# Performance work log

Hardware: AMD Instinct MI355X
Metric: run time of the kernel (lower is better)

## Reference

```python
import jax, jax.numpy as jnp
import numpy as np

# Tree config: batch of perfect binary trees in heap layout (root=0, children of i are 2i+1, 2i+2)
D_MODEL = 512
DEPTH = 10                      # number of internal levels
B = 64                          # number of trees in the batch
VOCAB = 32000
N_LEAVES = 2 ** DEPTH           # 1024 leaves per tree
N_NODES = 2 ** (DEPTH + 1) - 1  # 2047 nodes per tree
N_CLASSES = 2                   # binary graph classification


def setup_inputs() -> dict:
    key = jax.random.key(0)
    k_tok, k_emb, k_iou, k_f, k_out = jax.random.split(key, 5)
    d = D_MODEL
    s_in = 1.0 / np.sqrt(2 * d)
    return {
        "tokens": jax.random.randint(k_tok, (B, N_LEAVES), 0, VOCAB, dtype=jnp.int32),
        "embedding": (jax.random.normal(k_emb, (VOCAB, d), jnp.float32) * 0.02),
        "W_iou": jax.random.normal(k_iou, (2 * d, 3 * d), jnp.float32) * s_in,
        "b_iou": jnp.zeros((3 * d,), jnp.float32),
        "W_f": jax.random.normal(k_f, (2 * d, 2 * d), jnp.float32) * s_in,
        "b_f": jnp.zeros((2 * d,), jnp.float32),
        "W_out": jax.random.normal(k_out, (d, N_CLASSES), jnp.float32) * (1.0 / np.sqrt(d)),
    }


def reference(tokens, embedding, W_iou, b_iou, W_f, b_f, W_out):
    # Shared activation / memory buffers over all nodes, as in RecursiveNN.forward.
    d = embedding.shape[1]
    b = tokens.shape[0]
    h = jnp.zeros((b, N_NODES, d), jnp.float32)   # activations
    c = jnp.zeros((b, N_NODES, d), jnp.float32)   # memory (memory_size=1)

    # Leaves: embedding lookup, scattered into the activation buffer.
    leaf_h = embedding[tokens]                    # [B, N_LEAVES, d]
    h = h.at[:, N_LEAVES - 1:].set(leaf_h)

    # Internal nodes by topological level (leaf-adjacent level first, root last).
    for level in range(DEPTH - 1, -1, -1):
        idx = np.arange(2 ** level - 1, 2 ** (level + 1) - 1)  # node group (static)
        left, right = 2 * idx + 1, 2 * idx + 2                 # predecessor indices
        # Gather predecessor activations and memory.
        hl, hr = h[:, left], h[:, right]                       # [B, n, d]
        cl, cr = c[:, left], c[:, right]
        x = jnp.concatenate([hl, hr], axis=-1)                 # [B, n, 2d]
        # Binary TreeLSTM cell (the _apply_function for the 'add' binary op).
        iou = x @ W_iou + b_iou
        i, o, u = jnp.split(iou, 3, axis=-1)
        f = jax.nn.sigmoid(x @ W_f + b_f)
        fl, fr = jnp.split(f, 2, axis=-1)
        c_new = jax.nn.sigmoid(i) * jnp.tanh(u) + fl * cl + fr * cr
        h_new = jax.nn.sigmoid(o) * jnp.tanh(c_new)
        # Scatter back into the shared buffers.
        h = h.at[:, idx].set(h_new)
        c = c.at[:, idx].set(c_new)

    # _compute_output: linear binary-classification head on the root activation.
    return h[:, 0] @ W_out                                     # [B, N_CLASSES]
```

## Files before the change

kernel.cpp:

```cpp
#include <hip/hip_runtime.h>
#include <math.h>

typedef unsigned short u16;
typedef short s16x8 __attribute__((ext_vector_type(8)));
typedef float f32x4 __attribute__((ext_vector_type(4)));

#define NITER 32
#define ARW 72
#define BRW 72

__device__ __align__(16) u16 g_Bhi[1024 * 2560];
__device__ __align__(16) u16 g_Blo[1024 * 2560];

__device__ __forceinline__ u16 f2bf(float x) {
    unsigned u = __float_as_uint(x);
    u += 0x7fffu + ((u >> 16) & 1u);
    return (u16)(u >> 16);
}
__device__ __forceinline__ float bf2f(u16 h) { return __uint_as_float(((unsigned)h) << 16); }
__device__ __forceinline__ float sigm(float x) { return 1.0f / (1.0f + expf(-x)); }
__device__ __forceinline__ unsigned pk(u16 a, u16 b) { return (unsigned)a | ((unsigned)b << 16); }

__global__ __launch_bounds__(256)
void wsplit_kernel(const float* __restrict__ Wiou, const float* __restrict__ Wf)
{
    __shared__ float tile[32][65];
    const int kb = blockIdx.x;
    const int cb = blockIdx.y;
    const int t  = threadIdx.x;
    const int c0 = cb * 64;

    {
        const int kk  = t >> 3;
        const int cu0 = (t & 7) * 8;
        const int k   = kb * 32 + kk;
#pragma unroll
        for (int u = 0; u < 8; u++) {
            int c = c0 + cu0 + u;
            float v = (c < 1536) ? Wiou[(size_t)k * 1536 + c]
                                 : Wf[(size_t)k * 1024 + (c - 1536)];
            tile[kk][cu0 + u] = v;
        }
    }
    __syncthreads();
    {
        const int jl = t >> 2;
        const int kc = (t & 3) * 8;
        const int g  = c0 >> 9;
        const int j  = (c0 & 511) + jl;
        size_t dst = (((size_t)kb * 5 + g) * 512 + j) * 32 + kc;
        unsigned ph[4], pl[4];
#pragma unroll
        for (int u = 0; u < 4; u++) {
            float v0 = tile[kc + 2 * u][jl];
            float v1 = tile[kc + 2 * u + 1][jl];
            u16 h0 = f2bf(v0), h1 = f2bf(v1);
            u16 l0 = f2bf(v0 - bf2f(h0)), l1 = f2bf(v1 - bf2f(h1));
            ph[u] = pk(h0, h1);
            pl[u] = pk(l0, l1);
        }
        *(uint4*)(g_Bhi + dst) = make_uint4(ph[0], ph[1], ph[2], ph[3]);
        *(uint4*)(g_Blo + dst) = make_uint4(pl[0], pl[1], pl[2], pl[3]);
    }
}

template<bool LEAF>
__global__ __launch_bounds__(512, 2)
void level_mfma(const u16* __restrict__ Hc, const float* __restrict__ Cc,
                const int* __restrict__ tokens, const float* __restrict__ emb,
                const float* __restrict__ b_iou, const float* __restrict__ b_f,
                u16* __restrict__ Hp, float* __restrict__ Cp,
                int np, int lgnp)
{
    __shared__ __align__(16) u16 Ac[2][128 * ARW];
    __shared__ __align__(16) u16 Bc[2][320 * BRW];

    const int tid = threadIdx.x;
    const int jg  = blockIdx.x;
    const int m0  = blockIdx.y * 128;
    const int j0  = jg * 64;
    const int nc  = np * 2;
    const int M   = np * 64;

    const int w    = tid >> 6;
    const int lane = tid & 63;
    const int il   = lane & 15;
    const int kq   = lane >> 4;
    const int wm   = w & 1;
    const int wc   = w >> 1;

    f32x4 acc[4][5];
#pragma unroll
    for (int rf = 0; rf < 4; rf++)
#pragma unroll
        for (int g = 0; g < 5; g++) acc[rf][g] = (f32x4)0.0f;

    const int rA = tid >> 2;
    const int qA = tid & 3;
    int mA = m0 + rA; if (mA > M - 1) mA = M - 1;
    const int bA = mA >> lgnp;
    const int pA = mA & (np - 1);

    const u16* arow = nullptr;
    const float *erowL = nullptr, *erowR = nullptr;
    if (LEAF) {
        int tl = tokens[bA * 1024 + 2 * pA];
        int tr = tokens[bA * 1024 + 2 * pA + 1];
        erowL = emb + (size_t)tl * 512;
        erowR = emb + (size_t)tr * 512;
    } else {
        arow = Hc + ((size_t)bA * nc + 2 * pA) * 1024;
    }
    const int daI = rA * ARW + (qA & 1) * 32 + (qA >> 1) * 16;
    const int daL = rA * ARW + qA * 8;

    const int sB = tid & 7;
    const int cr = tid >> 3;
    const u16* bsel = (sB < 4) ? g_Bhi : g_Blo;
    const int soff = (sB & 3) * 8;
    const int dbB = cr * BRW + soff + (sB >> 2) * 32;

    uint4  aR0, aR1;
    float4 fR0, fR1;
    uint4  bR[5];

#define LOAD_TILE(t_)                                                          \
    {                                                                          \
        const int t__ = (t_);                                                  \
        if (LEAF) {                                                            \
            const float* asrc = ((t__ < 16) ? erowL : erowR)                   \
                                + ((32 * t__) & 511) + qA * 8;                 \
            fR0 = *(const float4*)asrc;                                        \
            fR1 = *(const float4*)(asrc + 4);                                  \
        } else {                                                               \
            const u16* asrc = arow + t__ * 64 + qA * 16;                       \
            aR0 = *(const uint4*)asrc;                                         \
            aR1 = *(const uint4*)(asrc + 8);                                   \
        }                                                                      \
        _Pragma("unroll")                                                      \
        for (int g = 0; g < 5; g++) {                                          \
            size_t off = (((size_t)t__ * 5 + g) * 512 + j0 + cr) * 32 + soff;  \
            bR[g] = *(const uint4*)(bsel + off);                               \
        }                                                                      \
    }

#define WRITE_TILE(bf)                                                         \
    {                                                                          \
        const int bf__ = (bf);                                                 \
        if (LEAF) {                                                            \
            float v[8] = {fR0.x, fR0.y, fR0.z, fR0.w, fR1.x, fR1.y, fR1.z, fR1.w}; \
            unsigned ph[4], pl[4];                                             \
            _Pragma("unroll")                                                  \
            for (int i = 0; i < 4; i++) {                                      \
                u16 h0 = f2bf(v[2 * i]), h1 = f2bf(v[2 * i + 1]);              \
                u16 l0 = f2bf(v[2 * i] - bf2f(h0));                            \
                u16 l1 = f2bf(v[2 * i + 1] - bf2f(h1));                        \
                ph[i] = pk(h0, h1);  pl[i] = pk(l0, l1);                       \
            }                                                                  \
            *(uint4*)&Ac[bf__][daL]      = make_uint4(ph[0], ph[1], ph[2], ph[3]); \
            *(uint4*)&Ac[bf__][daL + 32] = make_uint4(pl[0], pl[1], pl[2], pl[3]); \
        } else {                                                               \
            *(uint4*)&Ac[bf__][daI]     = aR0;                                 \
            *(uint4*)&Ac[bf__][daI + 8] = aR1;                                 \
        }                                                                      \
        _Pragma("unroll")                                                      \
        for (int g = 0; g < 5; g++)                                            \
            *(uint4*)&Bc[bf__][g * 64 * BRW + dbB] = bR[g];                    \
    }

    LOAD_TILE(0);
    WRITE_TILE(0);
    __syncthreads();

    int cur = 0;
    for (int t = 0; t < NITER; ++t) {
        const bool more = (t + 1 < NITER);
        if (more) LOAD_TILE(t + 1);

        {
            const u16* Acc_ = Ac[cur];
            const u16* Bcc_ = Bc[cur];
            s16x8 ahv[4], alv[4];
#pragma unroll
            for (int rf = 0; rf < 4; rf++) {
                const int ao = (wm * 64 + rf * 16 + il) * ARW + kq * 8;
                ahv[rf] = *(const s16x8*)&Acc_[ao];
                alv[rf] = *(const s16x8*)&Acc_[ao + 32];
            }
#pragma unroll
            for (int g = 0; g < 5; g++) {
                const int bo = (g * 64 + wc * 16 + il) * BRW + kq * 8;
                s16x8 bhv = *(const s16x8*)&Bcc_[bo];
                s16x8 blv = *(const s16x8*)&Bcc_[bo + 32];
#pragma unroll
                for (int rf = 0; rf < 4; rf++) {
                    acc[rf][g] = __builtin_amdgcn_mfma_f32_16x16x32_bf16(ahv[rf], bhv, acc[rf][g], 0, 0, 0);
                    acc[rf][g] = __builtin_amdgcn_mfma_f32_16x16x32_bf16(ahv[rf], blv, acc[rf][g], 0, 0, 0);
                    acc[rf][g] = __builtin_amdgcn_mfma_f32_16x16x32_bf16(alv[rf], bhv, acc[rf][g], 0, 0, 0);
                }
            }
        }

        if (more) {
            WRITE_TILE(cur ^ 1);
            __syncthreads();
            cur ^= 1;
        }
    }
#undef LOAD_TILE
#undef WRITE_TILE

    const int jglob = j0 + wc * 16 + il;
    const float bi  = b_iou[jglob];
    const float bo_ = b_iou[512 + jglob];
    const float bu  = b_iou[1024 + jglob];
    const float bfl = b_f[jglob];
    const float bfr = b_f[512 + jglob];

#pragma unroll
    for (int rf = 0; rf < 4; rf++) {
#pragma unroll
        for (int r = 0; r < 4; r++) {
            const int m = m0 + wm * 64 + rf * 16 + kq * 4 + r;
            if (m < M) {
                const int b = m >> lgnp;
                const int p = m & (np - 1);
                float i_ = acc[rf][0][r] + bi;
                float o_ = acc[rf][1][r] + bo_;
                float u_ = acc[rf][2][r] + bu;
                float fl = sigm(acc[rf][3][r] + bfl);
                float fr = sigm(acc[rf][4][r] + bfr);
                float cl = 0.0f, cr_ = 0.0f;
                if (!LEAF) {
                    size_t cb_ = ((size_t)b * nc + 2 * p) * 512 + jglob;
                    cl  = Cc[cb_];
                    cr_ = Cc[cb_ + 512];
                }
                float cn = sigm(i_) * tanhf(u_) + fl * cl + fr * cr_;
                float hn = sigm(o_) * tanhf(cn);
                size_t prow = (size_t)b * np + p;
                u16 hh = f2bf(hn);
                u16 hlo = f2bf(hn - bf2f(hh));
                Hp[prow * 1024 + (size_t)(jg * 4 + wc) * 32 + il]      = hh;
                Hp[prow * 1024 + (size_t)(jg * 4 + wc) * 32 + 16 + il] = hlo;
                Cp[prow * 512 + jglob] = cn;
            }
        }
    }
}

__global__ __launch_bounds__(256)
void out_kernel(const u16* __restrict__ Hroot, const float* __restrict__ W_out,
                float* __restrict__ out)
{
    const int b = blockIdx.x;
    const int tid = threadIdx.x;
    float s0 = 0.f, s1 = 0.f;
    for (int d = tid; d < 512; d += 256) {
        const u16* row = Hroot + (size_t)b * 1024 + (d >> 4) * 32 + (d & 15);
        float h = bf2f(row[0]) + bf2f(row[16]);
        s0 = fmaf(h, W_out[d * 2 + 0], s0);
        s1 = fmaf(h, W_out[d * 2 + 1], s1);
    }
#pragma unroll
    for (int off = 32; off > 0; off >>= 1) {
        s0 += __shfl_down(s0, off, 64);
        s1 += __shfl_down(s1, off, 64);
    }
    __shared__ float red[2][4];
    const int wave = tid >> 6;
    if ((tid & 63) == 0) { red[0][wave] = s0; red[1][wave] = s1; }
    __syncthreads();
    if (tid == 0) {
        float t0 = 0.f, t1 = 0.f;
#pragma unroll
        for (int wv = 0; wv < 4; wv++) { t0 += red[0][wv]; t1 += red[1][wv]; }
        out[b * 2 + 0] = t0;
        out[b * 2 + 1] = t1;
    }
}

extern "C" void kernel_launch(void* const* d_in, const int* in_sizes, int n_in,
                              void* d_out, int out_size, void* d_ws, size_t ws_size,
                              hipStream_t stream)
{
    const int*   tokens = (const int*)  d_in[0];
    const float* emb    = (const float*)d_in[1];
    const float* W_iou  = (const float*)d_in[2];
    const float* b_iou  = (const float*)d_in[3];
    const float* W_f    = (const float*)d_in[4];
    const float* b_f    = (const float*)d_in[5];
    const float* W_out  = (const float*)d_in[6];
    float* out = (float*)d_out;

    u16*   H0 = (u16*)d_ws;
    float* C0 = (float*)(H0 + (size_t)512 * 64 * 1024);
    u16*   H1 = (u16*)(C0 + (size_t)512 * 64 * 512);
    float* C1 = (float*)(H1 + (size_t)256 * 64 * 1024);

    wsplit_kernel<<<dim3(32, 40), 256, 0, stream>>>(W_iou, W_f);

    level_mfma<true><<<dim3(8, 256), 512, 0, stream>>>(
        nullptr, nullptr, tokens, emb, b_iou, b_f, H0, C0, 512, 9);

    u16* Hc = H0;  float* Cc = C0;
    u16* Hp = H1;  float* Cp = C1;
    for (int L = 8; L >= 0; L--) {
        const int np = 1 << L;
        const int gy = (np * 64 + 127) / 128;
        level_mfma<false><<<dim3(8, gy), 512, 0, stream>>>(
            Hc, Cc, nullptr, nullptr, b_iou, b_f, Hp, Cp, np, L);
        u16* tH = Hc; Hc = Hp; Hp = tH;
        float* tC = Cc; Cc = Cp; Cp = tC;
    }

    out_kernel<<<64, 256, 0, stream>>>(Hc, W_out, out);
}
```

Before: 1.333 ms.

## Load weight fragments directly from global into registers, bypassing LDS

The B (weight) operand is no longer staged through shared memory. Each lane loads its MFMA fragments for the hi and lo bf16 splits straight from global memory into double-buffered registers, and the loop is unrolled by two to alternate between buffers. This removes the LDS traffic for B and frees a large share of shared memory, which may allow more blocks per CU. In exchange it raises register pressure and issues more, smaller global loads, since the two wave rows that share a column group now each fetch the same weights.

New measurement: 1.521 ms. 14.1% more time.

```diff
diff --git a/kernel.cpp b/kernel.cpp
--- a/kernel.cpp
+++ b/kernel.cpp
@@ -7,7 +7,6 @@
 
 #define NITER 32
 #define ARW 72
-#define BRW 72
 
 __device__ __align__(16) u16 g_Bhi[1024 * 2560];
 __device__ __align__(16) u16 g_Blo[1024 * 2560];
@@ -73,7 +72,6 @@
                 int np, int lgnp)
 {
     __shared__ __align__(16) u16 Ac[2][128 * ARW];
-    __shared__ __align__(16) u16 Bc[2][320 * BRW];
 
     const int tid = threadIdx.x;
     const int jg  = blockIdx.x;
@@ -114,17 +112,14 @@
     const int daI = rA * ARW + (qA & 1) * 32 + (qA >> 1) * 16;
     const int daL = rA * ARW + qA * 8;
 
-    const int sB = tid & 7;
-    const int cr = tid >> 3;
-    const u16* bsel = (sB < 4) ? g_Bhi : g_Blo;
-    const int soff = (sB & 3) * 8;
-    const int dbB = cr * BRW + soff + (sB >> 2) * 32;
+    const u16* bbH = g_Bhi + ((size_t)(j0 + wc * 16 + il)) * 32 + kq * 8;
+    const u16* bbL = g_Blo + ((size_t)(j0 + wc * 16 + il)) * 32 + kq * 8;
 
     uint4  aR0, aR1;
     float4 fR0, fR1;
-    uint4  bR[5];
-
-#define LOAD_TILE(t_)                                                          \
+    s16x8 b0h[5], b0l[5], b1h[5], b1l[5];
+
+#define LOADA(t_)                                                              \
     {                                                                          \
         const int t__ = (t_);                                                  \
         if (LEAF) {                                                            \
@@ -137,14 +132,19 @@
             aR0 = *(const uint4*)asrc;                                         \
             aR1 = *(const uint4*)(asrc + 8);                                   \
         }                                                                      \
+    }
+
+#define LOADB(BH, BL, t_)                                                      \
+    {                                                                          \
+        const size_t tb = (size_t)(t_) * 5 * 16384;                            \
         _Pragma("unroll")                                                      \
         for (int g = 0; g < 5; g++) {                                          \
-            size_t off = (((size_t)t__ * 5 + g) * 512 + j0 + cr) * 32 + soff;  \
-            bR[g] = *(const uint4*)(bsel + off);                               \
+            BH[g] = *(const s16x8*)(bbH + tb + (size_t)g * 16384);             \
+            BL[g] = *(const s16x8*)(bbL + tb + (size_t)g * 16384);             \
         }                                                                      \
     }
 
-#define WRITE_TILE(bf)                                                         \
+#define WRITEA(bf)                                                             \
     {                                                                          \
         const int bf__ = (bf);                                                 \
         if (LEAF) {                                                            \
@@ -163,52 +163,54 @@
             *(uint4*)&Ac[bf__][daI]     = aR0;                                 \
             *(uint4*)&Ac[bf__][daI + 8] = aR1;                                 \
         }                                                                      \
+    }
+
+#define COMPUTE(BH, BL, BUF)                                                   \
+    {                                                                          \
         _Pragma("unroll")                                                      \
-        for (int g = 0; g < 5; g++)                                            \
-            *(uint4*)&Bc[bf__][g * 64 * BRW + dbB] = bR[g];                    \
-    }
-
-    LOAD_TILE(0);
-    WRITE_TILE(0);
+        for (int rf = 0; rf < 4; rf++) {                                       \
+            const int ao = (wm * 64 + rf * 16 + il) * ARW + kq * 8;            \
+            s16x8 ahv = *(const s16x8*)&Ac[BUF][ao];                           \
+            s16x8 alv = *(const s16x8*)&Ac[BUF][ao + 32];                      \
+            _Pragma("unroll")                                                  \
+            for (int g = 0; g < 5; g++) {                                      \
+                acc[rf][g] = __builtin_amdgcn_mfma_f32_16x16x32_bf16(ahv, BH[g], acc[rf][g], 0, 0, 0); \
+                acc[rf][g] = __builtin_amdgcn_mfma_f32_16x16x32_bf16(ahv, BL[g], acc[rf][g], 0, 0, 0); \
+                acc[rf][g] = __builtin_amdgcn_mfma_f32_16x16x32_bf16(alv, BH[g], acc[rf][g], 0, 0, 0); \
+            }                                                                  \
+        }                                                                      \
+    }
+
+    LOADA(0);
+    LOADB(b0h, b0l, 0);
+    WRITEA(0);
     __syncthreads();
 
-    int cur = 0;
-    for (int t = 0; t < NITER; ++t) {
-        const bool more = (t + 1 < NITER);
-        if (more) LOAD_TILE(t + 1);
-
-        {
-            const u16* Acc_ = Ac[cur];
-            const u16* Bcc_ = Bc[cur];
-            s16x8 ahv[4], alv[4];
-#pragma unroll
-            for (int rf = 0; rf < 4; rf++) {
-                const int ao = (wm * 64 + rf * 16 + il) * ARW + kq * 8;
-                ahv[rf] = *(const s16x8*)&Acc_[ao];
-                alv[rf] = *(const s16x8*)&Acc_[ao + 32];
-            }
-#pragma unroll
-            for (int g = 0; g < 5; g++) {
-                const int bo = (g * 64 + wc * 16 + il) * BRW + kq * 8;
-                s16x8 bhv = *(const s16x8*)&Bcc_[bo];
-                s16x8 blv = *(const s16x8*)&Bcc_[bo + 32];
-#pragma unroll
-                for (int rf = 0; rf < 4; rf++) {
-                    acc[rf][g] = __builtin_amdgcn_mfma_f32_16x16x32_bf16(ahv[rf], bhv, acc[rf][g], 0, 0, 0);
-                    acc[rf][g] = __builtin_amdgcn_mfma_f32_16x16x32_bf16(ahv[rf], blv, acc[rf][g], 0, 0, 0);
-                    acc[rf][g] = __builtin_amdgcn_mfma_f32_16x16x32_bf16(alv[rf], bhv, acc[rf][g], 0, 0, 0);
-                }
-            }
-        }
-
-        if (more) {
-            WRITE_TILE(cur ^ 1);
+#pragma unroll 1
+    for (int t = 0; t < NITER; t += 2) {
+        if (t + 1 < NITER) {
+            LOADA(t + 1);
+            LOADB(b1h, b1l, t + 1);
+        }
+        COMPUTE(b0h, b0l, 0);
+        if (t + 1 < NITER) {
+            WRITEA(1);
             __syncthreads();
-            cur ^= 1;
-        }
-    }
-#undef LOAD_TILE
-#undef WRITE_TILE
+        }
+        if (t + 2 < NITER) {
+            LOADA(t + 2);
+            LOADB(b0h, b0l, t + 2);
+        }
+        COMPUTE(b1h, b1l, 1);
+        if (t + 2 < NITER) {
+            WRITEA(0);
+            __syncthreads();
+        }
+    }
+#undef LOADA
+#undef LOADB
+#undef WRITEA
+#undef COMPUTE
 
     const int jglob = j0 + wc * 16 + il;
     const float bi  = b_iou[jglob];
```
